# Kernel tuning notes

Hardware: AMD Instinct MI355X
Metric: run time of the kernel (lower is better)

The kernel has to match this reference:

```python
import jax, jax.numpy as jnp
import numpy as np

B, T, D = 4096, 200, 64
NEG_INF = jnp.float32(-2.0**32 + 1)


def setup_inputs() -> dict:
    key = jax.random.key(0)
    ks = jax.random.split(key, 8)
    return {
        "queries": jax.random.normal(ks[0], (B, D), dtype=jnp.float32),
        "keys": jax.random.normal(ks[1], (B, T, D), dtype=jnp.float32),
        "keys_length": jax.random.randint(ks[2], (B,), 0, T, dtype=jnp.int32),
        "W1": jax.random.normal(ks[3], (4 * D, 80), dtype=jnp.float32) * 0.05,
        "b1": jnp.zeros((80,), dtype=jnp.float32),
        "W2": jax.random.normal(ks[4], (80, 40), dtype=jnp.float32) * 0.05,
        "b2": jnp.zeros((40,), dtype=jnp.float32),
        "W3": jax.random.normal(ks[5], (40, 1), dtype=jnp.float32) * 0.05,
        "b3": jnp.zeros((1,), dtype=jnp.float32),
    }


def reference(queries, keys, keys_length, W1, b1, W2, b2, W3, b3):
    # queries: [B, D], keys: [B, T, D], keys_length: [B]
    q = jnp.broadcast_to(queries[:, None, :], keys.shape)  # tile over T
    din_all = jnp.concatenate([q, keys, q - keys, q * keys], axis=-1)  # [B, T, 4D]
    h = jax.nn.sigmoid(din_all @ W1 + b1)
    h = jax.nn.sigmoid(h @ W2 + b2)
    logits = (h @ W3 + b3)[..., 0]  # [B, T]
    # sequence mask: position t valid iff t < keys_length[b]
    mask = jnp.arange(keys.shape[1])[None, :] < keys_length[:, None]
    logits = jnp.where(mask, logits, NEG_INF)
    logits = logits / jnp.sqrt(jnp.float32(keys.shape[-1]))
    attn = jax.nn.softmax(logits, axis=-1)  # [B, T]
    out = jnp.einsum('bt,btd->bd', attn, keys)  # squeeze(matmul([B,1,T],[B,T,D]))
    return out
```

## Files before the change

### kernel.cpp

```cpp
#include <hip/hip_runtime.h>
#include <math.h>

constexpr int B_ = 4096, T_ = 200, D_ = 64, NT = 256;
constexpr float LOG2E = 1.4426950408889634f;

typedef __attribute__((ext_vector_type(8))) __bf16 bf16x8;
typedef __attribute__((ext_vector_type(4))) float f32x4;

__device__ __host__ inline unsigned short f2b_rne(float x) {
    unsigned u = __builtin_bit_cast(unsigned, x);
    u += 0x7FFF + ((u >> 16) & 1);
    return (unsigned short)(u >> 16);
}

__device__ inline unsigned short b16bits(float x) {
    return __builtin_bit_cast(unsigned short, (__bf16)x);
}

__device__ inline float frcp(float x) { return __builtin_amdgcn_rcpf(x); }

__device__ inline float fexp2(float x) {
#if __has_builtin(__builtin_amdgcn_exp2f)
    return __builtin_amdgcn_exp2f(x);
#else
    return exp2f(x);
#endif
}

__device__ inline bf16x8 pack8(float4 lo, float4 hi) {
    bf16x8 r;
    r[0] = (__bf16)lo.x; r[1] = (__bf16)lo.y; r[2] = (__bf16)lo.z; r[3] = (__bf16)lo.w;
    r[4] = (__bf16)hi.x; r[5] = (__bf16)hi.y; r[6] = (__bf16)hi.z; r[7] = (__bf16)hi.w;
    return r;
}

__global__ void fold_weights(const float* __restrict__ W1,
                             const float* __restrict__ W2,
                             unsigned short* __restrict__ w1f,
                             unsigned short* __restrict__ w2f,
                             unsigned short* __restrict__ wqff) {
    int i = blockIdx.x * blockDim.x + threadIdx.x;
    if (i < 10240) {
        int j = i & 7, lane = (i >> 3) & 63, nt = (i >> 9) % 5, s = i / 2560;
        int k = s * 32 + (lane >> 4) * 8 + j;
        int n = nt * 16 + (lane & 15);
        float v = (k < 64) ? W1[(64 + k) * 80 + n] - W1[(128 + k) * 80 + n]
                           : W1[(192 + (k - 64)) * 80 + n];
        w1f[i] = f2b_rne(v * LOG2E);
    } else if (i < 14848) {
        int i2 = i - 10240;
        int j = i2 & 7, lane = (i2 >> 3) & 63, nt = (i2 >> 9) % 3, s = i2 / 1536;
        int k = s * 32 + (lane >> 4) * 8 + j;
        int n = nt * 16 + (lane & 15);
        float v = (k < 80 && n < 40) ? W2[k * 40 + n] * LOG2E : 0.f;
        w2f[i2] = f2b_rne(v);
    } else if (i < 19968) {
        int i3 = i - 14848;
        int j = i3 & 7, lane = (i3 >> 3) & 63, nt = (i3 >> 9) % 5, s = i3 / 2560;
        int d = s * 32 + (lane >> 4) * 8 + j;
        int n = nt * 16 + (lane & 15);
        wqff[i3] = f2b_rne((W1[d * 80 + n] + W1[(128 + d) * 80 + n]) * LOG2E);
    }
}

__global__ __launch_bounds__(NT, 2)
void din_attn(const float* __restrict__ q, const float* __restrict__ keys,
              const int* __restrict__ klen,
              const unsigned short* __restrict__ w1f,
              const unsigned short* __restrict__ w2f,
              const unsigned short* __restrict__ wqff,
              const float* __restrict__ b1, const float* __restrict__ b2,
              const float* __restrict__ W3, const float* __restrict__ b3,
              float* __restrict__ out) {
    const int tid = threadIdx.x;
    const int l = tid & 63, wid = tid >> 6, g4 = l >> 4, ln = l & 15;
    const int b = blockIdx.x * 4 + wid;

    alignas(16) __shared__ unsigned short h1c[4][2][16 * 104];
    __shared__ float olds[4][64];

    const int len = klen[b];
    const int ntile = (len + 15) >> 4;
    const float* kb = keys + (size_t)b * 200 * 64;

    if (ntile == 0) {
        float4 oq = {0.f, 0.f, 0.f, 0.f};
        #pragma unroll 4
        for (int t = g4; t < 200; t += 4) {
            float4 kv = *(const float4*)(kb + t * 64 + 4 * ln);
            oq.x += kv.x; oq.y += kv.y; oq.z += kv.z; oq.w += kv.w;
        }
        oq.x += __shfl_xor(oq.x, 16); oq.x += __shfl_xor(oq.x, 32);
        oq.y += __shfl_xor(oq.y, 16); oq.y += __shfl_xor(oq.y, 32);
        oq.z += __shfl_xor(oq.z, 16); oq.z += __shfl_xor(oq.z, 32);
        oq.w += __shfl_xor(oq.w, 16); oq.w += __shfl_xor(oq.w, 32);
        if (g4 == 0) {
            oq.x *= 0.005f; oq.y *= 0.005f; oq.z *= 0.005f; oq.w *= 0.005f;
            *(float4*)(out + b * 64 + 4 * ln) = oq;
        }
        return;
    }

    unsigned short* buf0 = h1c[wid][0];
    unsigned short* buf1 = h1c[wid][1];
    #pragma unroll
    for (int r = 0; r < 4; ++r) {
        buf0[(g4 * 4 + r) * 104 + 80 + ln] = 0;
        buf1[(g4 * 4 + r) * 104 + 80 + ln] = 0;
    }

    const float b3v = b3[0];

#define LOADK(tile_, B0_, B1_, B2_, B3_) do {                              \
        int t_ = (tile_) * 16 + ln;                                        \
        int tc_ = t_ < 200 ? t_ : 199;                                     \
        const float* row_ = kb + tc_ * 64 + g4 * 8;                        \
        B0_ = *(const float4*)(row_);                                      \
        B1_ = *(const float4*)(row_ + 4);                                  \
        B2_ = *(const float4*)(row_ + 32);                                 \
        B3_ = *(const float4*)(row_ + 36);                                 \
    } while (0)

    float4 A0, A1, A2, A3, C0, C1, C2, C3;
    LOADK(0, A0, A1, A2, A3);
    LOADK(1, C0, C1, C2, C3);

    float b2v[3], w3v[3];
    #pragma unroll
    for (int nt = 0; nt < 3; ++nt) {
        int idx = nt * 16 + ln;
        b2v[nt] = (idx < 40) ? b2[idx] * LOG2E : 0.f;
        w3v[nt] = (idx < 40) ? W3[idx] : 0.f;
    }

    const float* qb = q + b * 64;
    float4 q0  = *(const float4*)(qb + g4 * 8);
    float4 q0b = *(const float4*)(qb + g4 * 8 + 4);
    float4 q1  = *(const float4*)(qb + 32 + g4 * 8);
    float4 q1b = *(const float4*)(qb + 32 + g4 * 8 + 4);
    bf16x8 qf0 = pack8(q0, q0b);
    bf16x8 qf1 = pack8(q1, q1b);

    float hv[5];
    {
        f32x4 hacc[5];
        #pragma unroll
        for (int nt = 0; nt < 5; ++nt) {
            float bv = b1[nt * 16 + ln] * LOG2E;
            hacc[nt] = (f32x4){bv, bv, bv, bv};
        }
        #pragma unroll
        for (int nt = 0; nt < 5; ++nt) {
            bf16x8 f0 = *(const bf16x8*)&wqff[((0 * 5 + nt) * 64 + l) * 8];
            bf16x8 f1 = *(const bf16x8*)&wqff[((1 * 5 + nt) * 64 + l) * 8];
            hacc[nt] = __builtin_amdgcn_mfma_f32_16x16x32_bf16(qf0, f0, hacc[nt], 0, 0, 0);
            hacc[nt] = __builtin_amdgcn_mfma_f32_16x16x32_bf16(qf1, f1, hacc[nt], 0, 0, 0);
        }
        #pragma unroll
        for (int nt = 0; nt < 5; ++nt) hv[nt] = hacc[nt][0];
    }

    bf16x8 wf_[2][5];
    #pragma unroll
    for (int s = 0; s < 2; ++s) {
        float qa0 = (s == 0) ? q0.x  : q1.x,  qa1 = (s == 0) ? q0.y  : q1.y;
        float qa2 = (s == 0) ? q0.z  : q1.z,  qa3 = (s == 0) ? q0.w  : q1.w;
        float qb0 = (s == 0) ? q0b.x : q1b.x, qb1 = (s == 0) ? q0b.y : q1b.y;
        float qb2 = (s == 0) ? q0b.z : q1b.z, qb3 = (s == 0) ? q0b.w : q1b.w;
        #pragma unroll
        for (int nt = 0; nt < 5; ++nt) {
            bf16x8 wk = *(const bf16x8*)&w1f[((s * 5 + nt) * 64 + l) * 8];
            bf16x8 wq = *(const bf16x8*)&w1f[(((s + 2) * 5 + nt) * 64 + l) * 8];
            bf16x8 r;
            r[0] = (__bf16)fmaf(qa0, (float)wq[0], (float)wk[0]);
            r[1] = (__bf16)fmaf(qa1, (float)wq[1], (float)wk[1]);
            r[2] = (__bf16)fmaf(qa2, (float)wq[2], (float)wk[2]);
            r[3] = (__bf16)fmaf(qa3, (float)wq[3], (float)wk[3]);
            r[4] = (__bf16)fmaf(qb0, (float)wq[4], (float)wk[4]);
            r[5] = (__bf16)fmaf(qb1, (float)wq[5], (float)wk[5]);
            r[6] = (__bf16)fmaf(qb2, (float)wq[6], (float)wk[6]);
            r[7] = (__bf16)fmaf(qb3, (float)wq[7], (float)wk[7]);
            wf_[s][nt] = r;
        }
    }

    float s_part = 0.f;
    float4 o0 = {0,0,0,0}, o1 = o0, o2 = o0, o3 = o0;
    float e0_, e1_, e2_, e3_;

#define L1SIG(K0_, K1_, K2_, K3_, DST_) do {                               \
        f32x4 acc[5];                                                      \
        _Pragma("unroll")                                                  \
        for (int nt = 0; nt < 5; ++nt)                                     \
            acc[nt] = (f32x4){hv[nt], hv[nt], hv[nt], hv[nt]};             \
        bf16x8 av0 = pack8(K0_, K1_);                                      \
        bf16x8 av1 = pack8(K2_, K3_);                                      \
        _Pragma("unroll")                                                  \
        for (int nt = 0; nt < 5; ++nt) {                                   \
            acc[nt] = __builtin_amdgcn_mfma_f32_16x16x32_bf16(             \
                av0, wf_[0][nt], acc[nt], 0, 0, 0);                        \
            acc[nt] = __builtin_amdgcn_mfma_f32_16x16x32_bf16(             \
                av1, wf_[1][nt], acc[nt], 0, 0, 0);                        \
        }                                                                  \
        _Pragma("unroll")                                                  \
        for (int nt = 0; nt < 5; ++nt)                                     \
            _Pragma("unroll")                                              \
            for (int r = 0; r < 4; ++r) {                                  \
                float sg = frcp(1.f + fexp2(-acc[nt][r]));                 \
                (DST_)[(g4 * 4 + r) * 104 + nt * 16 + ln] = b16bits(sg);   \
            }                                                              \
    } while (0)

#define AFREAD(SRC_) do {                                                  \
        af0 = *(const bf16x8*)((SRC_) + ln * 104 + g4 * 8);                \
        af1 = *(const bf16x8*)((SRC_) + ln * 104 + 32 + g4 * 8);           \
        af2 = *(const bf16x8*)((SRC_) + ln * 104 + 64 + g4 * 8);           \
    } while (0)

#define L3E(tile_, r_, ER_) do {                                           \
        float p_ = w3v[0] * frcp(1.f + fexp2(-acc2[0][r_]))                \
                 + w3v[1] * frcp(1.f + fexp2(-acc2[1][r_]))                \
                 + w3v[2] * frcp(1.f + fexp2(-acc2[2][r_]));               \
        p_ += __shfl_xor(p_, 1); p_ += __shfl_xor(p_, 2);                  \
        p_ += __shfl_xor(p_, 4); p_ += __shfl_xor(p_, 8);                  \
        int trow_ = (tile_) * 16 + g4 * 4 + (r_);                          \
        ER_ = (trow_ < len)                                                \
            ? fexp2((p_ + b3v) * (0.125f * LOG2E)) : 0.f;                  \
    } while (0)

#define L2L3E(tile_) do {                                                  \
        f32x4 acc2[3];                                                     \
        _Pragma("unroll")                                                  \
        for (int nt = 0; nt < 3; ++nt)                                     \
            acc2[nt] = (f32x4){b2v[nt], b2v[nt], b2v[nt], b2v[nt]};        \
        _Pragma("unroll")                                                  \
        for (int nt = 0; nt < 3; ++nt) {                                   \
            bf16x8 w0_ = *(const bf16x8*)(w2f + ((0 * 3 + nt) * 64 + l) * 8); \
            bf16x8 w1_ = *(const bf16x8*)(w2f + ((1 * 3 + nt) * 64 + l) * 8); \
            bf16x8 w2_ = *(const bf16x8*)(w2f + ((2 * 3 + nt) * 64 + l) * 8); \
            acc2[nt] = __builtin_amdgcn_mfma_f32_16x16x32_bf16(af0, w0_, acc2[nt], 0, 0, 0); \
            acc2[nt] = __builtin_amdgcn_mfma_f32_16x16x32_bf16(af1, w1_, acc2[nt], 0, 0, 0); \
            acc2[nt] = __builtin_amdgcn_mfma_f32_16x16x32_bf16(af2, w2_, acc2[nt], 0, 0, 0); \
        }                                                                  \
        L3E(tile_, 0, e0_); L3E(tile_, 1, e1_);                            \
        L3E(tile_, 2, e2_); L3E(tile_, 3, e3_);                            \
    } while (0)

#define UPDATE(K0_, K1_, K2_, K3_) do {                                    \
        s_part += (e0_ + e1_) + (e2_ + e3_);                               \
        int rr_ = ln & 3;                                                  \
        float em_ = rr_ == 0 ? e0_ : rr_ == 1 ? e1_                        \
                  : rr_ == 2 ? e2_ : e3_;                                  \
        float pm_ = __shfl(em_, ((ln >> 2) << 4) + rr_);                   \
        o0.x = fmaf(pm_, K0_.x, o0.x); o0.y = fmaf(pm_, K0_.y, o0.y);      \
        o0.z = fmaf(pm_, K0_.z, o0.z); o0.w = fmaf(pm_, K0_.w, o0.w);      \
        o1.x = fmaf(pm_, K1_.x, o1.x); o1.y = fmaf(pm_, K1_.y, o1.y);      \
        o1.z = fmaf(pm_, K1_.z, o1.z); o1.w = fmaf(pm_, K1_.w, o1.w);      \
        o2.x = fmaf(pm_, K2_.x, o2.x); o2.y = fmaf(pm_, K2_.y, o2.y);      \
        o2.z = fmaf(pm_, K2_.z, o2.z); o2.w = fmaf(pm_, K2_.w, o2.w);      \
        o3.x = fmaf(pm_, K3_.x, o3.x); o3.y = fmaf(pm_, K3_.y, o3.y);      \
        o3.z = fmaf(pm_, K3_.z, o3.z); o3.w = fmaf(pm_, K3_.w, o3.w);      \
    } while (0)

    bf16x8 af0, af1, af2;
    L1SIG(A0, A1, A2, A3, buf0);
    if (ntile > 1) {
        int it = 0;
        #pragma unroll 1
        while (it + 2 < ntile) {
            AFREAD(buf0);
            L1SIG(C0, C1, C2, C3, buf1);
            L2L3E(it);
            UPDATE(A0, A1, A2, A3);
            LOADK(it + 2, A0, A1, A2, A3);
            AFREAD(buf1);
            L1SIG(A0, A1, A2, A3, buf0);
            L2L3E(it + 1);
            UPDATE(C0, C1, C2, C3);
            LOADK(it + 3, C0, C1, C2, C3);
            it += 2;
        }
        if (ntile - it == 2) {
            AFREAD(buf0);
            L1SIG(C0, C1, C2, C3, buf1);
            L2L3E(it);
            UPDATE(A0, A1, A2, A3);
            AFREAD(buf1);
            L2L3E(it + 1);
            UPDATE(C0, C1, C2, C3);
        } else {
            AFREAD(buf0);
            L2L3E(it);
            UPDATE(A0, A1, A2, A3);
        }
    } else {
        AFREAD(buf0);
        L2L3E(0);
        UPDATE(A0, A1, A2, A3);
    }
#undef LOADK
#undef L1SIG
#undef AFREAD
#undef L3E
#undef L2L3E
#undef UPDATE

    float s_tot = s_part;
    s_tot += __shfl_xor(s_tot, 16);
    s_tot += __shfl_xor(s_tot, 32);
    const float inv = frcp(s_tot);

#define RED16(x_) { x_ += __shfl_xor(x_, 1); x_ += __shfl_xor(x_, 2);      \
                    x_ += __shfl_xor(x_, 4); x_ += __shfl_xor(x_, 8); }
    RED16(o0.x) RED16(o0.y) RED16(o0.z) RED16(o0.w)
    RED16(o1.x) RED16(o1.y) RED16(o1.z) RED16(o1.w)
    RED16(o2.x) RED16(o2.y) RED16(o2.z) RED16(o2.w)
    RED16(o3.x) RED16(o3.y) RED16(o3.z) RED16(o3.w)
#undef RED16
    if (ln == 0) {
        float* od = olds[wid];
        od[g4 * 8 + 0] = o0.x; od[g4 * 8 + 1] = o0.y;
        od[g4 * 8 + 2] = o0.z; od[g4 * 8 + 3] = o0.w;
        od[g4 * 8 + 4] = o1.x; od[g4 * 8 + 5] = o1.y;
        od[g4 * 8 + 6] = o1.z; od[g4 * 8 + 7] = o1.w;
        od[32 + g4 * 8 + 0] = o2.x; od[32 + g4 * 8 + 1] = o2.y;
        od[32 + g4 * 8 + 2] = o2.z; od[32 + g4 * 8 + 3] = o2.w;
        od[32 + g4 * 8 + 4] = o3.x; od[32 + g4 * 8 + 5] = o3.y;
        od[32 + g4 * 8 + 6] = o3.z; od[32 + g4 * 8 + 7] = o3.w;
    }
    out[b * 64 + l] = olds[wid][l] * inv;
}

extern "C" void kernel_launch(void* const* d_in, const int* in_sizes, int n_in,
                              void* d_out, int out_size, void* d_ws, size_t ws_size,
                              hipStream_t stream) {
    const float* q    = (const float*)d_in[0];
    const float* keys = (const float*)d_in[1];
    const int*   kl   = (const int*)d_in[2];
    const float* W1   = (const float*)d_in[3];
    const float* b1   = (const float*)d_in[4];
    const float* W2   = (const float*)d_in[5];
    const float* b2   = (const float*)d_in[6];
    const float* W3   = (const float*)d_in[7];
    const float* b3   = (const float*)d_in[8];

    unsigned short* w1f  = (unsigned short*)d_ws;
    unsigned short* w2f  = w1f + 10240;
    unsigned short* wqff = w2f + 4608;

    fold_weights<<<(19968 + 255) / 256, 256, 0, stream>>>(W1, W2, w1f, w2f, wqff);
    din_attn<<<B_ / 4, NT, 0, stream>>>(q, keys, kl, w1f, w2f, wqff, b1, b2,
                                        W3, b3, (float*)d_out);
}
```

Baseline: 56.09 us.

## Sort batch rows by key length and interleave them across wavefronts for load balance

Adds a single-block kernel that counting-sorts batch rows by keys_length in descending order. It then builds a row map so each block's four wavefronts take rows from different quartiles of the sorted order, with the quartile rotated per block. The main kernel reads its batch index through this map, so per-row work (proportional to length) is balanced within blocks and long rows are scheduled first. The cost is an extra serial single-block launch plus one indirection load per wavefront.

```diff
diff --git a/kernel.cpp b/kernel.cpp
--- a/kernel.cpp
+++ b/kernel.cpp
@@ -63,9 +63,39 @@
     }
 }
 
+__global__ __launch_bounds__(256)
+void build_rowmap(const int* __restrict__ klen, int* __restrict__ rowmap) {
+    __shared__ int cnt[200];
+    __shared__ int base[200];
+    __shared__ unsigned int off[200];
+    __shared__ short sorted_[B_];
+    const int tid = threadIdx.x;
+    if (tid < 200) { cnt[tid] = 0; off[tid] = 0; }
+    __syncthreads();
+    for (int i = tid; i < B_; i += 256)
+        atomicAdd(&cnt[klen[i]], 1);
+    __syncthreads();
+    if (tid == 0) {
+        int acc = 0;
+        for (int len = 199; len >= 0; --len) { base[len] = acc; acc += cnt[len]; }
+    }
+    __syncthreads();
+    for (int i = tid; i < B_; i += 256) {
+        int ln = klen[i];
+        int pos = base[ln] + (int)atomicAdd(&off[ln], 1u);
+        sorted_[pos] = (short)i;
+    }
+    __syncthreads();
+    for (int idx = tid; idx < B_; idx += 256) {
+        int i = idx >> 2, w = idx & 3;
+        int role = (w + (i >> 8)) & 3;
+        rowmap[idx] = (int)sorted_[i + 1024 * role];
+    }
+}
+
 __global__ __launch_bounds__(NT, 2)
 void din_attn(const float* __restrict__ q, const float* __restrict__ keys,
-              const int* __restrict__ klen,
+              const int* __restrict__ klen, const int* __restrict__ rowmap,
               const unsigned short* __restrict__ w1f,
               const unsigned short* __restrict__ w2f,
               const unsigned short* __restrict__ wqff,
@@ -74,7 +104,7 @@
               float* __restrict__ out) {
     const int tid = threadIdx.x;
     const int l = tid & 63, wid = tid >> 6, g4 = l >> 4, ln = l & 15;
-    const int b = blockIdx.x * 4 + wid;
+    const int b = rowmap[blockIdx.x * 4 + wid];
 
     alignas(16) __shared__ unsigned short h1c[4][2][16 * 104];
     __shared__ float olds[4][64];
@@ -347,8 +377,10 @@
     unsigned short* w1f  = (unsigned short*)d_ws;
     unsigned short* w2f  = w1f + 10240;
     unsigned short* wqff = w2f + 4608;
+    int* rowmap = (int*)((char*)d_ws + 49152);
 
     fold_weights<<<(19968 + 255) / 256, 256, 0, stream>>>(W1, W2, w1f, w2f, wqff);
-    din_attn<<<B_ / 4, NT, 0, stream>>>(q, keys, kl, w1f, w2f, wqff, b1, b2,
-                                        W3, b3, (float*)d_out);
-}
+    build_rowmap<<<1, 256, 0, stream>>>(kl, rowmap);
+    din_attn<<<B_ / 4, NT, 0, stream>>>(q, keys, kl, rowmap, w1f, w2f, wqff,
+                                        b1, b2, W3, b3, (float*)d_out);
+}
```

New measurement: 64.38 us. 1.15x slower.
